# Performance work log

Hardware: AMD Instinct MI355X
Metric: run time of the kernel (lower is better)

The kernel has to match this reference:

```python
import jax, jax.numpy as jnp
import numpy as np

D_MODEL = 1024
N_HEADS = 16
HEAD_DIM = D_MODEL // N_HEADS
D_FF = 4096
LN_EPS = 1e-5


def _layernorm(x, g, b):
    mu = jnp.mean(x, axis=-1, keepdims=True)
    var = jnp.var(x, axis=-1, keepdims=True)
    return (x - mu) * jax.lax.rsqrt(var + LN_EPS) * g + b


def setup_inputs() -> dict:
    key = jax.random.key(0)
    ks = jax.random.split(key, 10)
    s = 0.02
    return {
        "hidden_states": jax.random.normal(ks[0], (2, 2048, D_MODEL), dtype=jnp.float32),
        "qkv_w": jax.random.normal(ks[1], (3 * D_MODEL, D_MODEL), dtype=jnp.float32) * s,
        "qkv_b": jnp.zeros((3 * D_MODEL,), dtype=jnp.float32),
        "out_w": jax.random.normal(ks[2], (D_MODEL, D_MODEL), dtype=jnp.float32) * s,
        "out_b": jnp.zeros((D_MODEL,), dtype=jnp.float32),
        "fc1_w": jax.random.normal(ks[3], (D_FF, D_MODEL), dtype=jnp.float32) * s,
        "fc1_b": jnp.zeros((D_FF,), dtype=jnp.float32),
        "fc2_w": jax.random.normal(ks[4], (D_MODEL, D_FF), dtype=jnp.float32) * s,
        "fc2_b": jnp.zeros((D_MODEL,), dtype=jnp.float32),
        "ln1_g": jnp.ones((D_MODEL,), dtype=jnp.float32),
        "ln1_b": jnp.zeros((D_MODEL,), dtype=jnp.float32),
        "ln2_g": jnp.ones((D_MODEL,), dtype=jnp.float32),
        "ln2_b": jnp.zeros((D_MODEL,), dtype=jnp.float32),
    }


def reference(hidden_states, qkv_w, qkv_b, out_w, out_b, fc1_w, fc1_b, fc2_w, fc2_b, ln1_g, ln1_b, ln2_g, ln2_b):
    B, S, D = hidden_states.shape
    scale = 1.0 / np.sqrt(HEAD_DIM).astype(np.float32)

    normed = _layernorm(hidden_states, ln1_g, ln1_b)
    qkv = normed @ qkv_w.T + qkv_b  # [B,S,3D]
    qkv = qkv.reshape(B, S, 3, N_HEADS, HEAD_DIM).transpose(2, 0, 3, 1, 4)
    q, k, v = qkv[0], qkv[1], qkv[2]  # [B,H,S,hd]

    scores = jnp.einsum("bhqd,bhkd->bhqk", q, k) * scale
    causal = jnp.tril(jnp.ones((S, S), dtype=bool))
    scores = jnp.where(causal, scores, jnp.float32(-jnp.inf))
    probs = jax.nn.softmax(scores, axis=-1)
    attn = jnp.einsum("bhqk,bhkd->bhqd", probs, v)  # [B,H,S,hd]
    attn = attn.transpose(0, 2, 1, 3).reshape(B, S, D)
    attn = attn @ out_w.T + out_b

    hidden = hidden_states + attn
    normed2 = _layernorm(hidden, ln2_g, ln2_b)
    ff = jax.nn.gelu(normed2 @ fc1_w.T + fc1_b, approximate=False)
    ff = ff @ fc2_w.T + fc2_b
    return hidden + ff
```

## Files before the change

### kernel.cpp

```cpp
#include <hip/hip_runtime.h>
#include <math.h>

using bf16   = __bf16;
using bf16x8 = __attribute__((ext_vector_type(8))) __bf16;
using bf16x4 = __attribute__((ext_vector_type(4))) __bf16;
using f32x4  = __attribute__((ext_vector_type(4))) float;
using f32x16 = __attribute__((ext_vector_type(16))) float;

#define MFMA_16x16x32(a, b, c) __builtin_amdgcn_mfma_f32_16x16x32_bf16((a), (b), (c), 0, 0, 0)
#define MFMA32(a, b, c) __builtin_amdgcn_mfma_f32_32x32x16_bf16((a), (b), (c), 0, 0, 0)

__device__ __forceinline__ void gll16(const void* g, void* l) {
  __builtin_amdgcn_global_load_lds((const __attribute__((address_space(1))) void*)g,
                                   (__attribute__((address_space(3))) void*)l,
                                   16, 0, 0);
}

__device__ __forceinline__ int cvtpk(float lo, float hi) {
  int r;
  asm("v_cvt_pk_bf16_f32 %0, %1, %2" : "=v"(r) : "v"(lo), "v"(hi));
  return r;
}

__global__ __launch_bounds__(256) void cast4_kernel(const float* __restrict__ s0, bf16* d0,
                                                    const float* __restrict__ s1, bf16* d1,
                                                    const float* __restrict__ s2, bf16* d2,
                                                    const float* __restrict__ s3, bf16* d3) {
  int i = blockIdx.x * 256 + threadIdx.x;
  const float* s;
  bf16* d;
  if (i < 786432) { s = s0; d = d0; }
  else if (i < 1048576) { s = s1; d = d1; i -= 786432; }
  else if (i < 2097152) { s = s2; d = d2; i -= 1048576; }
  else { s = s3; d = d3; i -= 2097152; }
  float4 v = ((const float4*)s)[i];
  bf16x4 o;
  o[0] = (bf16)v.x; o[1] = (bf16)v.y; o[2] = (bf16)v.z; o[3] = (bf16)v.w;
  ((bf16x4*)d)[i] = o;
}

__global__ __launch_bounds__(256) void ln_kernel(const float* __restrict__ x,
                                                 const float* __restrict__ g,
                                                 const float* __restrict__ b,
                                                 bf16* __restrict__ out) {
  const int row = blockIdx.x, t = threadIdx.x;
  const float4 v = ((const float4*)(x + (size_t)row * 1024))[t];
  float s1 = v.x + v.y + v.z + v.w;
  float s2 = v.x * v.x + v.y * v.y + v.z * v.z + v.w * v.w;
#pragma unroll
  for (int d = 32; d; d >>= 1) {
    s1 += __shfl_xor(s1, d);
    s2 += __shfl_xor(s2, d);
  }
  __shared__ float red[8];
  const int w = t >> 6;
  if ((t & 63) == 0) { red[w] = s1; red[4 + w] = s2; }
  __syncthreads();
  s1 = red[0] + red[1] + red[2] + red[3];
  s2 = red[4] + red[5] + red[6] + red[7];
  const float mu = s1 * (1.f / 1024.f);
  const float rstd = rsqrtf(s2 * (1.f / 1024.f) - mu * mu + 1e-5f);
  const float4 gv = ((const float4*)g)[t];
  const float4 bv = ((const float4*)b)[t];
  bf16x4 o;
  o[0] = (bf16)((v.x - mu) * rstd * gv.x + bv.x);
  o[1] = (bf16)((v.y - mu) * rstd * gv.y + bv.y);
  o[2] = (bf16)((v.z - mu) * rstd * gv.z + bv.z);
  o[3] = (bf16)((v.w - mu) * rstd * gv.w + bv.w);
  ((bf16x4*)(out + (size_t)row * 1024))[t] = o;
}

template <int EPI>
__global__ __launch_bounds__(512, 2) void gemm256(const bf16* __restrict__ A,
                                                  const bf16* __restrict__ W,
                                                  const float* __restrict__ bias,
                                                  bf16* __restrict__ outp, int N, int K,
                                                  int nbx) {
  __shared__ __align__(1024) bf16 lds[65536];
  const int t = threadIdx.x, lane = t & 63, w = t >> 6;
  const int wm = w >> 2, wn = w & 3;
  const int l15 = lane & 15, lg = lane >> 4;

  const int nwg = gridDim.x, cpx = nwg >> 3, bid = blockIdx.x;
  const int swz = (bid & 7) * cpx + (bid >> 3);
  const int bx = swz % nbx, by = swz / nbx;
  const int m0 = by * 256, n0 = bx * 256;

  const bf16* src[8];
  int dst[8];
  {
    const int ss[2] = {t, t + 512};
#pragma unroll
    for (int i = 0; i < 2; i++) {
      const int d = ss[i] * 16;
      const int L = d ^ (((d >> 9) & 1) << 5);
      const int r = L >> 7, coff = (L & 127) >> 1;
#pragma unroll
      for (int hf = 0; hf < 2; hf++) {
        src[hf * 2 + i]     = A + (size_t)(m0 + hf * 128 + r) * K + coff;
        src[4 + hf * 2 + i] = W + (size_t)(n0 + hf * 128 + r) * K + coff;
        dst[hf * 2 + i]     = hf * 8192 + ss[i] * 8;
        dst[4 + hf * 2 + i] = 16384 + hf * 8192 + ss[i] * 8;
      }
    }
  }

#define STAGE256(db_)                                   \
  do {                                                  \
    _Pragma("unroll") for (int u = 0; u < 8; u++) {     \
      gll16(src[u], lds + (db_)*32768 + dst[u]);        \
      src[u] += 64;                                     \
    }                                                   \
  } while (0)

  f32x4 acc[8][4];
#pragma unroll
  for (int mi = 0; mi < 8; mi++)
#pragma unroll
    for (int ni = 0; ni < 4; ni++) acc[mi][ni] = (f32x4){0.f, 0.f, 0.f, 0.f};

  const int ntiles = K >> 6;
  STAGE256(0);
  asm volatile("s_waitcnt vmcnt(0)" ::: "memory");
  __builtin_amdgcn_s_barrier();

  for (int kt = 0; kt < ntiles; ++kt) {
    const int db = kt & 1;
    const bf16* Ab = lds + db * 32768 + wm * 8192;
    const bf16* Bb = lds + db * 32768 + 16384 + (wn >> 1) * 8192;
    bf16x8 bfr[4][2];
#pragma unroll
    for (int p = 0; p < 4; ++p) {
      bf16x8 af[2][2];
#pragma unroll
      for (int mi2 = 0; mi2 < 2; ++mi2)
#pragma unroll
        for (int ks = 0; ks < 2; ++ks) {
          const int row = (2 * p + mi2) * 16 + l15;
          const int Pb = (row * 128 + ks * 64 + lg * 16) ^ (((row >> 2) & 1) << 5);
          af[mi2][ks] = *(const bf16x8*)((const char*)Ab + Pb);
        }
      if (p == 0) {
#pragma unroll
        for (int ni = 0; ni < 4; ++ni)
#pragma unroll
          for (int ks = 0; ks < 2; ++ks) {
            const int row = (wn & 1) * 64 + ni * 16 + l15;
            const int Pb = (row * 128 + ks * 64 + lg * 16) ^ (((row >> 2) & 1) << 5);
            bfr[ni][ks] = *(const bf16x8*)((const char*)Bb + Pb);
          }
        if (kt + 1 < ntiles) STAGE256(db ^ 1);
      }
      __builtin_amdgcn_s_barrier();
      asm volatile("s_waitcnt lgkmcnt(0)" ::: "memory");
      __builtin_amdgcn_sched_barrier(0);
      __builtin_amdgcn_s_setprio(1);
#pragma unroll
      for (int ks = 0; ks < 2; ++ks)
#pragma unroll
        for (int ni = 0; ni < 4; ++ni) {
          acc[2 * p][ni] = MFMA_16x16x32(af[0][ks], bfr[ni][ks], acc[2 * p][ni]);
          acc[2 * p + 1][ni] = MFMA_16x16x32(af[1][ks], bfr[ni][ks], acc[2 * p + 1][ni]);
        }
      __builtin_amdgcn_s_setprio(0);
      if (p == 3) asm volatile("s_waitcnt vmcnt(0)" ::: "memory");
      __builtin_amdgcn_s_barrier();
    }
  }
#undef STAGE256

#pragma unroll
  for (int mi = 0; mi < 8; ++mi) {
    const int row0 = m0 + wm * 128 + mi * 16 + lg * 4;
#pragma unroll
    for (int ni = 0; ni < 4; ++ni) {
      const int col = n0 + wn * 64 + ni * 16 + l15;
      const float bc = bias[col];
#pragma unroll
      for (int r = 0; r < 4; ++r) {
        float v = acc[mi][ni][r] + bc;
        if (EPI == 1) v = 0.5f * v * (1.f + erff(v * 0.70710678118f));
        outp[(size_t)(row0 + r) * N + col] = (bf16)v;
      }
    }
  }
}

__global__ __launch_bounds__(512, 2) void gemm128(const bf16* __restrict__ A,
                                                  const bf16* __restrict__ W,
                                                  const float* __restrict__ bias,
                                                  const float* __restrict__ resid,
                                                  float* __restrict__ outp, int N, int K,
                                                  int nbx) {
  __shared__ __align__(1024) bf16 lds[65536];
  const int t = threadIdx.x, lane = t & 63, w = t >> 6;
  const int wm = w >> 2, wn = w & 3;
  const int l15 = lane & 15, lg = lane >> 4;

  const int nwg = gridDim.x, cpx = nwg >> 3, bid = blockIdx.x;
  const int swz = (bid & 7) * cpx + (bid >> 3);
  const int bx = swz % nbx, by = swz / nbx;
  const int m0 = by * 128, n0 = bx * 128;

  const bf16* src[8];
  int dst[8];
#pragma unroll
  for (int i = 0; i < 4; i++) {
    const int off = i * 8192 + t * 16;
    const int row = off >> 8, slot = (off >> 4) & 15;
    const int col = (slot ^ (row & 7)) * 8;
    src[i]     = A + (size_t)(m0 + row) * K + col;
    src[4 + i] = W + (size_t)(n0 + row) * K + col;
    dst[i]     = off >> 1;
    dst[4 + i] = 16384 + (off >> 1);
  }

#define STAGE128(db_)                                   \
  do {                                                  \
    _Pragma("unroll") for (int u = 0; u < 8; u++) {     \
      gll16(src[u], lds + (db_)*32768 + dst[u]);        \
      src[u] += 128;                                    \
    }                                                   \
  } while (0)

  f32x4 acc[4][2];
#pragma unroll
  for (int mi = 0; mi < 4; mi++)
#pragma unroll
    for (int ni = 0; ni < 2; ni++) acc[mi][ni] = (f32x4){0.f, 0.f, 0.f, 0.f};

  const int ntiles = K >> 7;
  STAGE128(0);
  asm volatile("s_waitcnt vmcnt(0)" ::: "memory");
  __builtin_amdgcn_s_barrier();

  for (int kt = 0; kt < ntiles; ++kt) {
    const int db = kt & 1;
    const char* Ab = (const char*)(lds + db * 32768);
    const char* Bb = (const char*)(lds + db * 32768 + 16384);
#pragma unroll
    for (int p = 0; p < 4; ++p) {
      bf16x8 af[4], bfr[2];
#pragma unroll
      for (int mi = 0; mi < 4; ++mi) {
        const int row = wm * 64 + mi * 16 + l15;
        af[mi] = *(const bf16x8*)(Ab + row * 256 + (((p * 4 + lg) ^ (row & 7)) << 4));
      }
#pragma unroll
      for (int ni = 0; ni < 2; ++ni) {
        const int row = wn * 32 + ni * 16 + l15;
        bfr[ni] = *(const bf16x8*)(Bb + row * 256 + (((p * 4 + lg) ^ (row & 7)) << 4));
      }
      if (p == 0 && kt + 1 < ntiles) STAGE128(db ^ 1);
      __builtin_amdgcn_s_barrier();
      asm volatile("s_waitcnt lgkmcnt(0)" ::: "memory");
      __builtin_amdgcn_sched_barrier(0);
      __builtin_amdgcn_s_setprio(1);
#pragma unroll
      for (int mi = 0; mi < 4; ++mi)
#pragma unroll
        for (int ni = 0; ni < 2; ++ni)
          acc[mi][ni] = MFMA_16x16x32(af[mi], bfr[ni], acc[mi][ni]);
      __builtin_amdgcn_s_setprio(0);
      if (p == 3) asm volatile("s_waitcnt vmcnt(0)" ::: "memory");
      __builtin_amdgcn_s_barrier();
    }
  }
#undef STAGE128

#pragma unroll
  for (int mi = 0; mi < 4; ++mi) {
    const int row0 = m0 + wm * 64 + mi * 16 + lg * 4;
#pragma unroll
    for (int ni = 0; ni < 2; ++ni) {
      const int col = n0 + wn * 32 + ni * 16 + l15;
      const float bc = bias[col];
#pragma unroll
      for (int r = 0; r < 4; ++r) {
        const size_t idx = (size_t)(row0 + r) * N + col;
        outp[idx] = acc[mi][ni][r] + bc + resid[idx];
      }
    }
  }
}

__global__ __launch_bounds__(256) void vtrans_kernel(const bf16* __restrict__ qkv,
                                                     bf16* __restrict__ vt) {
  __shared__ bf16 tile[64 * 80];
  const int bh = blockIdx.y, b = bh >> 4, h = bh & 15;
  const int s0 = blockIdx.x * 64;
  const int t = threadIdx.x;
#pragma unroll
  for (int c = t; c < 512; c += 256) {
    const int s = c >> 3, d0 = (c & 7) * 8;
    const bf16x8 v =
        *(const bf16x8*)(qkv + (size_t)(b * 2048 + s0 + s) * 3072 + 2048 + h * 64 + d0);
#pragma unroll
    for (int i = 0; i < 8; i++) {
      const int d = d0 + i;
      tile[d * 80 + (s ^ (8 * ((d >> 3) & 7)))] = v[i];
    }
  }
  __syncthreads();
#pragma unroll
  for (int c = t; c < 512; c += 256) {
    const int d = c >> 3, sc = (c & 7) * 8;
    const bf16x8 v = *(const bf16x8*)&tile[d * 80 + (sc ^ (8 * ((d >> 3) & 7)))];
    *(bf16x8*)(vt + ((size_t)bh * 64 + d) * 2048 + s0 + sc) = v;
  }
}

__global__ __launch_bounds__(256) void attn_kernel(const bf16* __restrict__ qkv,
                                                   const bf16* __restrict__ vt,
                                                   bf16* __restrict__ attn_out) {
  __shared__ bf16 Ks[2][4096];
  __shared__ bf16 Vs[2][4096];
  const int t = threadIdx.x, lane = t & 63, w = t >> 6;
  const int l31 = lane & 31, lh = lane >> 5;
  const int bx = blockIdx.x, by = blockIdx.y;
  const int b = by >> 4, h = by & 15;
  const int g = (bx + by) & 15;
  const int qb = (by < 16) ? g : 15 - g;
  const int qw = qb * 128 + w * 32;
  const int qq = qw + l31;
  const int nt = 2 * qb + 2;

  const float cs = 0.18033688011112042f;

  bf16x8 qf[4];
  {
    const bf16* qp = qkv + (size_t)(b * 2048 + qq) * 3072 + h * 64 + lh * 8;
#pragma unroll
    for (int c = 0; c < 4; ++c) qf[c] = *(const bf16x8*)(qp + c * 16);
  }

  const int r0 = t >> 3, c16 = t & 7;
  const int swsl = 8 * (c16 ^ (r0 & 7));
  const bf16* kp0 = qkv + (size_t)(b * 2048 + r0) * 3072 + 1024 + h * 64 + swsl;
  const bf16* kp1 = qkv + (size_t)(b * 2048 + r0 + 32) * 3072 + 1024 + h * 64 + swsl;
  const bf16* vp0 = vt + ((size_t)by * 64 + r0) * 2048 + swsl;
  const bf16* vp1 = vp0 + (size_t)32 * 2048;

#define ASTAGE(buf)                          \
  do {                                       \
    gll16(kp0, &Ks[buf][t * 8]);             \
    gll16(kp1, &Ks[buf][2048 + t * 8]);      \
    gll16(vp0, &Vs[buf][t * 8]);             \
    gll16(vp1, &Vs[buf][2048 + t * 8]);      \
    kp0 += (size_t)64 * 3072;                \
    kp1 += (size_t)64 * 3072;                \
    vp0 += 64;                               \
    vp1 += 64;                               \
  } while (0)

  const f32x16 z16 = {0.f, 0.f, 0.f, 0.f, 0.f, 0.f, 0.f, 0.f,
                      0.f, 0.f, 0.f, 0.f, 0.f, 0.f, 0.f, 0.f};
  f32x16 oacc0 = z16, oacc1 = z16;
  float m = -1e30f, lsum = 0.f;

  ASTAGE(0);
  __syncthreads();
  int cur = 0;
  for (int tt = 0; tt < nt; ++tt) {
    const int kv0 = tt * 64;
    if (tt + 1 < nt) ASTAGE(cur ^ 1);
    if (kv0 <= qw + 31) {
      const bf16* kbp = Ks[cur];
      const bf16* vbp = Vs[cur];
      f32x16 s0v = z16, s1v = z16;
#pragma unroll
      for (int c = 0; c < 4; ++c) {
        const int slot = ((c * 2 + lh) ^ (l31 & 7)) * 16;
        const bf16x8 a0 = *(const bf16x8*)((const char*)kbp + l31 * 128 + slot);
        const bf16x8 a1 = *(const bf16x8*)((const char*)kbp + (32 + l31) * 128 + slot);
        s0v = MFMA32(a0, qf[c], s0v);
        s1v = MFMA32(a1, qf[c], s1v);
      }
      if (kv0 + 64 > qw) {
#pragma unroll
        for (int j = 0; j < 16; ++j) {
          const int kr = kv0 + (j & 3) + 8 * (j >> 2) + 4 * lh;
          if (kr > qq) s0v[j] = -1e30f;
          if (kr + 32 > qq) s1v[j] = -1e30f;
        }
      }
      float mx = -1e30f;
#pragma unroll
      for (int j = 0; j < 16; ++j) mx = fmaxf(mx, fmaxf(s0v[j], s1v[j]));
      mx = fmaxf(mx, __shfl_xor(mx, 32));
      const float mn = fmaxf(m, mx);
      const float alpha = exp2f((m - mn) * cs);
      m = mn;
      const float mcs = mn * cs;
      float rs = 0.f;
#pragma unroll
      for (int j = 0; j < 16; ++j) {
        s0v[j] = exp2f(__builtin_fmaf(s0v[j], cs, -mcs));
        s1v[j] = exp2f(__builtin_fmaf(s1v[j], cs, -mcs));
        rs += s0v[j] + s1v[j];
      }
      rs += __shfl_xor(rs, 32);
      lsum = lsum * alpha + rs;
#pragma unroll
      for (int j = 0; j < 16; ++j) { oacc0[j] *= alpha; oacc1[j] *= alpha; }
      int w0[8], w1[8], x0[8], x1[8];
#pragma unroll
      for (int j = 0; j < 8; ++j) {
        w0[j] = cvtpk(s0v[2 * j], s0v[2 * j + 1]);
        w1[j] = cvtpk(s1v[2 * j], s1v[2 * j + 1]);
      }
#pragma unroll
      for (int j = 0; j < 8; ++j) {
        x0[j] = __shfl_xor(w0[j], 32);
        x1[j] = __shfl_xor(w1[j], 32);
      }
#define PVHALF(WW, XX, KB)                                                        \
  do {                                                                            \
    _Pragma("unroll") for (int cc = 0; cc < 2; ++cc) {                            \
      union { int i[4]; bf16x8 v; } pf;                                           \
      pf.i[0] = lh ? XX[4 * cc + 2] : WW[4 * cc + 0];                             \
      pf.i[1] = lh ? XX[4 * cc + 3] : WW[4 * cc + 1];                             \
      pf.i[2] = lh ? WW[4 * cc + 2] : XX[4 * cc + 0];                             \
      pf.i[3] = lh ? WW[4 * cc + 3] : XX[4 * cc + 1];                             \
      const int slot = (((KB)*4 + cc * 2 + lh) ^ (l31 & 7)) * 16;                 \
      const bf16x8 v0 = *(const bf16x8*)((const char*)vbp + l31 * 128 + slot);    \
      const bf16x8 v1 = *(const bf16x8*)((const char*)vbp + (32 + l31) * 128 + slot); \
      oacc0 = MFMA32(v0, pf.v, oacc0);                                            \
      oacc1 = MFMA32(v1, pf.v, oacc1);                                            \
    }                                                                             \
  } while (0)
      PVHALF(w0, x0, 0);
      PVHALF(w1, x1, 1);
#undef PVHALF
    }
    __syncthreads();
    cur ^= 1;
  }
#undef ASTAGE

  const float rinv = 1.f / lsum;
  bf16* op = attn_out + (size_t)(b * 2048 + qq) * 1024 + h * 64;
#pragma unroll
  for (int gR = 0; gR < 4; ++gR) {
    bf16x4 o0, o1;
#pragma unroll
    for (int r = 0; r < 4; ++r) {
      o0[r] = (bf16)(oacc0[4 * gR + r] * rinv);
      o1[r] = (bf16)(oacc1[4 * gR + r] * rinv);
    }
    *(bf16x4*)(op + 8 * gR + 4 * lh) = o0;
    *(bf16x4*)(op + 32 + 8 * gR + 4 * lh) = o1;
  }
}

extern "C" void kernel_launch(void* const* d_in, const int* in_sizes, int n_in,
                              void* d_out, int out_size, void* d_ws, size_t ws_size,
                              hipStream_t stream) {
  (void)in_sizes; (void)n_in; (void)out_size; (void)ws_size;
  const float* hidden = (const float*)d_in[0];
  const float* qkv_w  = (const float*)d_in[1];
  const float* qkv_b  = (const float*)d_in[2];
  const float* out_w  = (const float*)d_in[3];
  const float* out_b  = (const float*)d_in[4];
  const float* fc1_w  = (const float*)d_in[5];
  const float* fc1_b  = (const float*)d_in[6];
  const float* fc2_w  = (const float*)d_in[7];
  const float* fc2_b  = (const float*)d_in[8];
  const float* ln1_g  = (const float*)d_in[9];
  const float* ln1_b  = (const float*)d_in[10];
  const float* ln2_g  = (const float*)d_in[11];
  const float* ln2_b  = (const float*)d_in[12];
  float* outp = (float*)d_out;

  char* ws = (char*)d_ws;
  bf16*  ln1o = (bf16*)(ws);
  bf16*  qkvb = (bf16*)(ws + ((size_t)8 << 20));
  bf16*  vtb  = (bf16*)(ws + ((size_t)32 << 20));
  bf16*  atto = (bf16*)(ws + ((size_t)40 << 20));
  float* res1 = (float*)(ws + ((size_t)48 << 20));
  bf16*  ln2o = (bf16*)(ws + ((size_t)64 << 20));
  bf16*  ff1  = (bf16*)(ws + ((size_t)72 << 20));
  bf16*  wqkv = (bf16*)(ws + ((size_t)104 << 20));
  bf16*  wout = (bf16*)(ws + ((size_t)110 << 20));
  bf16*  wfc1 = (bf16*)(ws + ((size_t)112 << 20));
  bf16*  wfc2 = (bf16*)(ws + ((size_t)120 << 20));

  cast4_kernel<<<12288, 256, 0, stream>>>(qkv_w, wqkv, out_w, wout, fc1_w, wfc1, fc2_w, wfc2);

  ln_kernel<<<4096, 256, 0, stream>>>(hidden, ln1_g, ln1_b, ln1o);
  gemm256<0><<<192, 512, 0, stream>>>(ln1o, wqkv, qkv_b, qkvb, 3072, 1024, 12);
  vtrans_kernel<<<dim3(32, 32), 256, 0, stream>>>(qkvb, vtb);
  attn_kernel<<<dim3(16, 32), 256, 0, stream>>>(qkvb, vtb, atto);
  gemm128<<<256, 512, 0, stream>>>(atto, wout, out_b, hidden, res1, 1024, 1024, 8);
  ln_kernel<<<4096, 256, 0, stream>>>(res1, ln2_g, ln2_b, ln2o);
  gemm256<1><<<256, 512, 0, stream>>>(ln2o, wfc1, fc1_b, ff1, 4096, 1024, 16);
  gemm128<<<256, 512, 0, stream>>>(ff1, wfc2, fc2_b, res1, outp, 1024, 4096, 8);
}
```

Baseline: 261.6 us.

## Shrink attention blocks to 64 queries, skip masked KV halves, lazy rescale

The attention kernel now uses 128-thread blocks, each owning 64 query rows, and launches twice as many blocks. On a diagonal tile, a wave skips the upper 32-row half of the KV tile when it is fully masked for that wave, avoiding its QK and PV MFMAs and its exp work. The running max and accumulator rescale only happen when the new max exceeds the old by more than a threshold, and s_setprio is raised around the MFMA sections. Risks: each K/V tile is loaded and shared by fewer waves, so reuse per load drops, and the lazy rescale relies on bounded exponent growth for accuracy.

```diff
diff --git a/kernel.cpp b/kernel.cpp
--- a/kernel.cpp
+++ b/kernel.cpp
@@ -310,7 +310,7 @@
   }
 }
 
-__global__ __launch_bounds__(256) void attn_kernel(const bf16* __restrict__ qkv,
+__global__ __launch_bounds__(128) void attn_kernel(const bf16* __restrict__ qkv,
                                                    const bf16* __restrict__ vt,
                                                    bf16* __restrict__ attn_out) {
   __shared__ bf16 Ks[2][4096];
@@ -319,11 +319,10 @@
   const int l31 = lane & 31, lh = lane >> 5;
   const int bx = blockIdx.x, by = blockIdx.y;
   const int b = by >> 4, h = by & 15;
-  const int g = (bx + by) & 15;
-  const int qb = (by < 16) ? g : 15 - g;
-  const int qw = qb * 128 + w * 32;
+  const int qb = (bx + by) & 31;
+  const int qw = qb * 64 + w * 32;
   const int qq = qw + l31;
-  const int nt = 2 * qb + 2;
+  const int nt = qb + 1;
 
   const float cs = 0.18033688011112042f;
 
@@ -334,23 +333,27 @@
     for (int c = 0; c < 4; ++c) qf[c] = *(const bf16x8*)(qp + c * 16);
   }
 
-  const int r0 = t >> 3, c16 = t & 7;
-  const int swsl = 8 * (c16 ^ (r0 & 7));
-  const bf16* kp0 = qkv + (size_t)(b * 2048 + r0) * 3072 + 1024 + h * 64 + swsl;
-  const bf16* kp1 = qkv + (size_t)(b * 2048 + r0 + 32) * 3072 + 1024 + h * 64 + swsl;
-  const bf16* vp0 = vt + ((size_t)by * 64 + r0) * 2048 + swsl;
-  const bf16* vp1 = vp0 + (size_t)32 * 2048;
-
-#define ASTAGE(buf)                          \
-  do {                                       \
-    gll16(kp0, &Ks[buf][t * 8]);             \
-    gll16(kp1, &Ks[buf][2048 + t * 8]);      \
-    gll16(vp0, &Vs[buf][t * 8]);             \
-    gll16(vp1, &Vs[buf][2048 + t * 8]);      \
-    kp0 += (size_t)64 * 3072;                \
-    kp1 += (size_t)64 * 3072;                \
-    vp0 += 64;                               \
-    vp1 += 64;                               \
+  const bf16* ksrc[4];
+  const bf16* vsrc[4];
+  int doff[4];
+#pragma unroll
+  for (int u = 0; u < 4; ++u) {
+    const int c = t + 128 * u;
+    const int row = c >> 3;
+    const int sl = 8 * ((c & 7) ^ (row & 7));
+    ksrc[u] = qkv + (size_t)(b * 2048 + row) * 3072 + 1024 + h * 64 + sl;
+    vsrc[u] = vt + ((size_t)by * 64 + row) * 2048 + sl;
+    doff[u] = c * 8;
+  }
+
+#define ASTAGE(buf)                              \
+  do {                                           \
+    _Pragma("unroll") for (int u = 0; u < 4; ++u) { \
+      gll16(ksrc[u], &Ks[buf][doff[u]]);         \
+      gll16(vsrc[u], &Vs[buf][doff[u]]);         \
+      ksrc[u] += (size_t)64 * 3072;              \
+      vsrc[u] += 64;                             \
+    }                                            \
   } while (0)
 
   const f32x16 z16 = {0.f, 0.f, 0.f, 0.f, 0.f, 0.f, 0.f, 0.f,
@@ -367,15 +370,24 @@
     if (kv0 <= qw + 31) {
       const bf16* kbp = Ks[cur];
       const bf16* vbp = Vs[cur];
+      const bool up = (kv0 + 32) <= (qw + 31);
       f32x16 s0v = z16, s1v = z16;
+      __builtin_amdgcn_s_setprio(1);
 #pragma unroll
       for (int c = 0; c < 4; ++c) {
         const int slot = ((c * 2 + lh) ^ (l31 & 7)) * 16;
         const bf16x8 a0 = *(const bf16x8*)((const char*)kbp + l31 * 128 + slot);
-        const bf16x8 a1 = *(const bf16x8*)((const char*)kbp + (32 + l31) * 128 + slot);
         s0v = MFMA32(a0, qf[c], s0v);
-        s1v = MFMA32(a1, qf[c], s1v);
-      }
+      }
+      if (up) {
+#pragma unroll
+        for (int c = 0; c < 4; ++c) {
+          const int slot = ((c * 2 + lh) ^ (l31 & 7)) * 16;
+          const bf16x8 a1 = *(const bf16x8*)((const char*)kbp + (32 + l31) * 128 + slot);
+          s1v = MFMA32(a1, qf[c], s1v);
+        }
+      }
+      __builtin_amdgcn_s_setprio(0);
       if (kv0 + 64 > qw) {
 #pragma unroll
         for (int j = 0; j < 16; ++j) {
@@ -385,35 +397,43 @@
         }
       }
       float mx = -1e30f;
-#pragma unroll
-      for (int j = 0; j < 16; ++j) mx = fmaxf(mx, fmaxf(s0v[j], s1v[j]));
+      if (up) {
+#pragma unroll
+        for (int j = 0; j < 16; ++j) mx = fmaxf(mx, fmaxf(s0v[j], s1v[j]));
+      } else {
+#pragma unroll
+        for (int j = 0; j < 16; ++j) mx = fmaxf(mx, s0v[j]);
+      }
       mx = fmaxf(mx, __shfl_xor(mx, 32));
-      const float mn = fmaxf(m, mx);
-      const float alpha = exp2f((m - mn) * cs);
-      m = mn;
-      const float mcs = mn * cs;
+      if (!__all(mx <= m + 44.36f)) {
+        const float mn = fmaxf(m, mx);
+        const float alpha = exp2f((m - mn) * cs);
+        m = mn;
+        lsum *= alpha;
+#pragma unroll
+        for (int j = 0; j < 16; ++j) { oacc0[j] *= alpha; oacc1[j] *= alpha; }
+      }
+      const float mcs = m * cs;
       float rs = 0.f;
 #pragma unroll
       for (int j = 0; j < 16; ++j) {
         s0v[j] = exp2f(__builtin_fmaf(s0v[j], cs, -mcs));
-        s1v[j] = exp2f(__builtin_fmaf(s1v[j], cs, -mcs));
-        rs += s0v[j] + s1v[j];
+        rs += s0v[j];
+      }
+      if (up) {
+#pragma unroll
+        for (int j = 0; j < 16; ++j) {
+          s1v[j] = exp2f(__builtin_fmaf(s1v[j], cs, -mcs));
+          rs += s1v[j];
+        }
       }
       rs += __shfl_xor(rs, 32);
-      lsum = lsum * alpha + rs;
-#pragma unroll
-      for (int j = 0; j < 16; ++j) { oacc0[j] *= alpha; oacc1[j] *= alpha; }
-      int w0[8], w1[8], x0[8], x1[8];
-#pragma unroll
-      for (int j = 0; j < 8; ++j) {
-        w0[j] = cvtpk(s0v[2 * j], s0v[2 * j + 1]);
-        w1[j] = cvtpk(s1v[2 * j], s1v[2 * j + 1]);
-      }
-#pragma unroll
-      for (int j = 0; j < 8; ++j) {
-        x0[j] = __shfl_xor(w0[j], 32);
-        x1[j] = __shfl_xor(w1[j], 32);
-      }
+      lsum += rs;
+      int w0[8], x0[8];
+#pragma unroll
+      for (int j = 0; j < 8; ++j) w0[j] = cvtpk(s0v[2 * j], s0v[2 * j + 1]);
+#pragma unroll
+      for (int j = 0; j < 8; ++j) x0[j] = __shfl_xor(w0[j], 32);
 #define PVHALF(WW, XX, KB)                                                        \
   do {                                                                            \
     _Pragma("unroll") for (int cc = 0; cc < 2; ++cc) {                            \
@@ -429,8 +449,19 @@
       oacc1 = MFMA32(v1, pf.v, oacc1);                                            \
     }                                                                             \
   } while (0)
+      __builtin_amdgcn_s_setprio(1);
       PVHALF(w0, x0, 0);
-      PVHALF(w1, x1, 1);
+      __builtin_amdgcn_s_setprio(0);
+      if (up) {
+        int w1[8], x1[8];
+#pragma unroll
+        for (int j = 0; j < 8; ++j) w1[j] = cvtpk(s1v[2 * j], s1v[2 * j + 1]);
+#pragma unroll
+        for (int j = 0; j < 8; ++j) x1[j] = __shfl_xor(w1[j], 32);
+        __builtin_amdgcn_s_setprio(1);
+        PVHALF(w1, x1, 1);
+        __builtin_amdgcn_s_setprio(0);
+      }
 #undef PVHALF
     }
     __syncthreads();
@@ -490,7 +521,7 @@
   ln_kernel<<<4096, 256, 0, stream>>>(hidden, ln1_g, ln1_b, ln1o);
   gemm256<0><<<192, 512, 0, stream>>>(ln1o, wqkv, qkv_b, qkvb, 3072, 1024, 12);
   vtrans_kernel<<<dim3(32, 32), 256, 0, stream>>>(qkvb, vtb);
-  attn_kernel<<<dim3(16, 32), 256, 0, stream>>>(qkvb, vtb, atto);
+  attn_kernel<<<dim3(32, 32), 128, 0, stream>>>(qkvb, vtb, atto);
   gemm128<<<256, 512, 0, stream>>>(atto, wout, out_b, hidden, res1, 1024, 1024, 8);
   ln_kernel<<<4096, 256, 0, stream>>>(res1, ln2_g, ln2_b, ln2o);
   gemm256<1><<<256, 512, 0, stream>>>(ln2o, wfc1, fc1_b, ff1, 4096, 1024, 16);
```

After: 273.7 us. +4.6%, slower.
